# Performance work log

Hardware: AMD Instinct MI355X
Metric: run time of the kernel (lower is better)

The kernel has to match this reference:

```python
import jax, jax.numpy as jnp
import numpy as np

TEMPERATURE = 0.1
B, T, D = 8, 1024, 1024
NEG_INF = -1e30

def setup_inputs() -> dict:
    key = jax.random.key(0)
    k1, k2, k3 = jax.random.split(key, 3)
    features = jax.random.normal(k1, (B, T, D), dtype=jnp.float32)
    masks = jax.random.bernoulli(k2, 0.05, (B, 1, T, T)).astype(jnp.float32)
    input_coords_length = jax.random.randint(k3, (B,), T // 2, T - 1)  # int32
    return {"features": features, "masks": masks, "input_coords_length": input_coords_length}


def _sup_con_loss(feat, mask, L):
    # feat: [T, D], mask: [T, T] float, L: scalar int valid length (slice [:L, :L])
    Tn = feat.shape[0]
    dt = feat.dtype
    vr = jnp.arange(Tn) < L                              # valid rows/cols [T]
    valid2d = (vr[:, None] & vr[None, :]).astype(dt)     # [T, T]
    dot = jnp.matmul(feat, feat.T) / TEMPERATURE         # [T, T]
    dot = jnp.where(vr[None, :], dot, NEG_INF)           # exclude padded cols from max
    logits = dot - jax.lax.stop_gradient(jnp.max(dot, axis=-1, keepdims=True))
    logits_mask = (1.0 - jnp.eye(Tn, dtype=dt)) * valid2d  # off-diagonal, in-slice
    exp_logits = jnp.exp(logits) * logits_mask
    m = mask * valid2d
    # negative_mask = 1-mask; entries < 1 zeroed (binary mask -> indicator of mask==0)
    neg = 1.0 - m
    neg = jnp.where(neg < 1.0, 0.0, neg) * valid2d
    # positive_mask = mask with entries > 0 set to 1
    pos = jnp.where(m > 0, 1.0, m)
    neg_denom = jnp.sum(exp_logits * neg, axis=-1, keepdims=True)
    pos_denom = jax.lax.stop_gradient(jnp.sum(exp_logits * pos, axis=-1, keepdims=True))
    log_prob = logits - jnp.log(neg_denom + pos_denom + 1e-6)
    m2 = m * logits_mask
    mean_log_prob_pos = (m2 * log_prob).sum(-1) / (m2.sum(-1) + 1e-6)  # [T]
    # mean over the L valid rows only (matches .mean() on the sliced tensor)
    return -jnp.sum(jnp.where(vr, mean_log_prob_pos, 0.0)) / L.astype(dt)


def _is_valid(mask, L):
    # valid sample iff sliced mask differs from eye(L) with [0,0]=0
    Tn = mask.shape[0]
    vr = jnp.arange(Tn) < L
    valid2d = (vr[:, None] & vr[None, :]).astype(mask.dtype)
    sanity = jnp.eye(Tn, dtype=mask.dtype).at[0, 0].set(0.0) * valid2d
    return jnp.any((mask * valid2d) != sanity)


def reference(features, masks, input_coords_length):
    L = input_coords_length + 1                      # [B]
    mask0 = masks[:, 0]                              # [B, T, T] (num_layers asserted == 1)
    losses = jax.vmap(_sup_con_loss)(features, mask0, L)   # [B]
    valid = jax.vmap(_is_valid)(mask0, L)                  # [B] bool
    vbs = jnp.maximum(jnp.sum(valid.astype(features.dtype)), 1.0)
    return jnp.sum(losses) / vbs
```

## Files before the change

kernel.cpp:

```cpp
#include <hip/hip_runtime.h>
#include <hip/hip_bf16.h>
#include <stdint.h>

#define T_DIM 1024
#define B_DIM 8

typedef __attribute__((ext_vector_type(8))) short short8;
typedef __attribute__((ext_vector_type(4))) float f32x4;

__device__ inline void gll16(const void* g, void* l) {
  __builtin_amdgcn_global_load_lds((__attribute__((address_space(1))) void*)g,
                                   (__attribute__((address_space(3))) void*)l,
                                   16, 0, 0);
}

__global__ __launch_bounds__(256) void convert_kernel(const float* __restrict__ F,
                                                      __hip_bfloat16* __restrict__ Fb) {
  const int t = blockIdx.x * 256 + threadIdx.x;
  const float4 v = ((const float4*)F)[t];
  union { __hip_bfloat16 h[4]; uint64_t u; } p;
  p.h[0] = __float2bfloat16(v.x);
  p.h[1] = __float2bfloat16(v.y);
  p.h[2] = __float2bfloat16(v.z);
  p.h[3] = __float2bfloat16(v.w);
  ((uint64_t*)Fb)[t] = p.u;
}

__global__ __launch_bounds__(512, 4) void fused_kernel(const __hip_bfloat16* __restrict__ Fb,
                                                       const float* __restrict__ M,
                                                       const int* __restrict__ icl,
                                                       float* __restrict__ part) {
  const int id = blockIdx.x;
  const int b  = id & 7;
  const int rt = (id >> 3) & 7;
  const int ct = id >> 6;
  const int L  = icl[b] + 1;
  if (rt * 128 >= L || ct * 128 >= L) return;

  __shared__ char smem[65536];
  __hip_bfloat16* As = (__hip_bfloat16*)smem;
  __hip_bfloat16* Bs = (__hip_bfloat16*)(smem + 32768);
  float* rp = (float*)smem;
  float* rp_m = rp;
  float* rp_d = rp + 512;
  float* rp_s = rp + 1024;
  float* rp_c = rp + 1536;
  float* rp_b = rp + 2048;

  const __hip_bfloat16* F = Fb + ((size_t)b << 20);
  const int tid  = threadIdx.x;
  const int lane = tid & 63;
  const int wave = tid >> 6;
  const int wrow = (wave >> 2) * 64;
  const int wcol = (wave & 3) * 32;
  const int row0 = rt * 128;
  const int col0 = ct * 128;
  const bool diag = (rt == ct);

  const int fr = lane & 15;
  const int q  = lane >> 4;
  const int sl8 = (q ^ ((fr >> 1) & 3)) * 8;

  const int srow = tid >> 2;
  const int sgk  = (((tid & 3) ^ ((tid >> 3) & 3)) * 8);

  const int gc0 = col0 + wcol + fr;
  const int gc1 = gc0 + 16;

  uint32_t mbits = 0;
  {
    const float* Mb = M + ((size_t)b << 20);
#pragma unroll
    for (int ti = 0; ti < 4; ti++)
#pragma unroll
      for (int r = 0; r < 4; r++) {
        const int grow = row0 + wrow + ti * 16 + q * 4 + r;
        const float* mrow = Mb + ((size_t)grow << 10);
        const uint32_t b0 = (gc0 < L && mrow[gc0] != 0.f) ? 1u : 0u;
        const uint32_t b1 = (gc1 < L && mrow[gc1] != 0.f) ? 1u : 0u;
        mbits |= (b0 << (ti * 8 + r * 2)) | (b1 << (ti * 8 + r * 2 + 1));
      }
  }

  f32x4 acc[4][2];
#pragma unroll
  for (int i = 0; i < 4; i++)
#pragma unroll
    for (int j = 0; j < 2; j++) acc[i][j] = (f32x4){0.f, 0.f, 0.f, 0.f};

  const size_t arow = (size_t)(row0 + srow) * T_DIM + sgk;
  const size_t brow = (size_t)(col0 + srow) * T_DIM + sgk;

  auto stage = [&](int buf, int step) {
    const int kb = step << 6;
#pragma unroll
    for (int p = 0; p < 2; p++)
      gll16(F + arow + kb + p * 32, As + buf * 8192 + p * 4096 + tid * 8);
    if (!diag) {
#pragma unroll
      for (int p = 0; p < 2; p++)
        gll16(F + brow + kb + p * 32, Bs + buf * 8192 + p * 4096 + tid * 8);
    }
  };

  stage(0, 0);
  __syncthreads();

#pragma unroll 2
  for (int t = 0; t < 16; t++) {
    const int cur = t & 1;
    if (t < 15) stage(cur ^ 1, t + 1);
#pragma unroll
    for (int kk = 0; kk < 2; kk++) {
      const __hip_bfloat16* Ab = As + cur * 8192 + kk * 4096;
      const __hip_bfloat16* Bb = diag ? Ab : (Bs + cur * 8192 + kk * 4096);
      short8 af[4], bfr[2];
#pragma unroll
      for (int tt = 0; tt < 4; tt++)
        af[tt] = *(const short8*)(Ab + (wrow + tt * 16 + fr) * 32 + sl8);
#pragma unroll
      for (int j = 0; j < 2; j++)
        bfr[j] = *(const short8*)(Bb + (wcol + j * 16 + fr) * 32 + sl8);
#pragma unroll
      for (int ti = 0; ti < 4; ti++)
#pragma unroll
        for (int tj = 0; tj < 2; tj++)
          acc[ti][tj] = __builtin_amdgcn_mfma_f32_16x16x32_bf16(af[ti], bfr[tj], acc[ti][tj], 0, 0, 0);
    }
    __syncthreads();
  }

#pragma unroll
  for (int ti = 0; ti < 4; ti++) {
#pragma unroll
    for (int r = 0; r < 4; r++) {
      const int lrow = wrow + ti * 16 + q * 4 + r;
      const int grow = row0 + lrow;
      const float mk0 = (float)((mbits >> (ti * 8 + r * 2)) & 1u);
      const float mk1 = (float)((mbits >> (ti * 8 + r * 2 + 1)) & 1u);
      const float s0 = (gc0 < L) ? acc[ti][0][r] * 10.0f : -1e30f;
      const float s1 = (gc1 < L) ? acc[ti][1][r] * 10.0f : -1e30f;
      float m = fmaxf(s0, s1);
#pragma unroll
      for (int d = 1; d < 16; d <<= 1) m = fmaxf(m, __shfl_xor(m, d, 64));
      float den = 0.f, msum = 0.f, cnt = 0.f, badf = 0.f;
      if (gc0 < L) {
        if (gc0 != grow) { den += __expf(s0 - m); msum += mk0 * s0; cnt += mk0; }
        const float sane = (gc0 == grow && grow != 0) ? 1.f : 0.f;
        badf = fmaxf(badf, (mk0 != sane) ? 1.f : 0.f);
      }
      if (gc1 < L) {
        if (gc1 != grow) { den += __expf(s1 - m); msum += mk1 * s1; cnt += mk1; }
        const float sane = (gc1 == grow && grow != 0) ? 1.f : 0.f;
        badf = fmaxf(badf, (mk1 != sane) ? 1.f : 0.f);
      }
#pragma unroll
      for (int d = 1; d < 16; d <<= 1) {
        den  += __shfl_xor(den, d, 64);
        msum += __shfl_xor(msum, d, 64);
        cnt  += __shfl_xor(cnt, d, 64);
        badf  = fmaxf(badf, __shfl_xor(badf, d, 64));
      }
      if (fr == 0) {
        const int slot = wave & 3;
        rp_m[lrow * 4 + slot] = m;   rp_d[lrow * 4 + slot] = den;
        rp_s[lrow * 4 + slot] = msum; rp_c[lrow * 4 + slot] = cnt;
        rp_b[lrow * 4 + slot] = badf;
      }
    }
  }
  __syncthreads();

  if (tid < 128) {
    float m = -1e30f;
#pragma unroll
    for (int s = 0; s < 4; s++) m = fmaxf(m, rp_m[tid * 4 + s]);
    float den = 0.f, msum = 0.f, cnt = 0.f, badf = 0.f;
#pragma unroll
    for (int s = 0; s < 4; s++) {
      den  += rp_d[tid * 4 + s] * __expf(rp_m[tid * 4 + s] - m);
      msum += rp_s[tid * 4 + s];
      cnt  += rp_c[tid * 4 + s];
      badf  = fmaxf(badf, rp_b[tid * 4 + s]);
    }
    float* p = part + ((((size_t)b * 1024 + row0 + tid) * 8) + ct) * 5;
    p[0] = m; p[1] = den; p[2] = msum; p[3] = cnt; p[4] = badf;
  }
}

__global__ __launch_bounds__(256) void reduce_kernel(const float* __restrict__ part,
                                                     const int* __restrict__ icl,
                                                     float* __restrict__ blk_sum,
                                                     int* __restrict__ blk_bad) {
  const int blk = blockIdx.x;
  const int row = blk * 256 + threadIdx.x;
  const int b = row >> 10;
  const int i = row & 1023;
  const int L = icl[b] + 1;
  float rv = 0.f;
  int bad = 0;
  if (i < L) {
    const float* p = part + (size_t)row * 40;
    const int ns = (L + 127) >> 7;
    float m = -1e30f;
    for (int s = 0; s < ns; s++) m = fmaxf(m, p[s * 5 + 0]);
    float den = 0.f, msum = 0.f, cnt = 0.f, badf = 0.f;
    for (int s = 0; s < ns; s++) {
      den  += p[s * 5 + 1] * __expf(p[s * 5 + 0] - m);
      msum += p[s * 5 + 2];
      cnt  += p[s * 5 + 3];
      badf  = fmaxf(badf, p[s * 5 + 4]);
    }
    const float A = msum - cnt * m;
    const float mlpp = (A - cnt * __logf(den + 1e-6f)) / (cnt + 1e-6f);
    rv = -mlpp / (float)L;
    bad = badf > 0.f ? 1 : 0;
  }
  const int tid  = threadIdx.x;
  const int lane = tid & 63;
  const int wave = tid >> 6;
  for (int o = 32; o > 0; o >>= 1) rv += __shfl_down(rv, o, 64);
  const int wbad = (__ballot(bad) != 0ull) ? 1 : 0;
  __shared__ float sred[4];
  __shared__ int bred[4];
  if (lane == 0) { sred[wave] = rv; bred[wave] = wbad; }
  __syncthreads();
  if (tid == 0) {
    blk_sum[blk] = sred[0] + sred[1] + sred[2] + sred[3];
    blk_bad[blk] = bred[0] | bred[1] | bred[2] | bred[3];
  }
}

__global__ __launch_bounds__(64) void final_kernel(const float* __restrict__ blk_sum,
                                                   const int* __restrict__ blk_bad,
                                                   float* __restrict__ out) {
  const int tid = threadIdx.x;
  float v = (tid < 32) ? blk_sum[tid] : 0.f;
  for (int o = 32; o > 0; o >>= 1) v += __shfl_down(v, o, 64);
  if (tid == 0) {
    int vcount = 0;
    for (int bb = 0; bb < B_DIM; bb++) {
      const int any = blk_bad[bb * 4] | blk_bad[bb * 4 + 1] |
                      blk_bad[bb * 4 + 2] | blk_bad[bb * 4 + 3];
      vcount += any ? 1 : 0;
    }
    out[0] = v / fmaxf((float)vcount, 1.0f);
  }
}

extern "C" void kernel_launch(void* const* d_in, const int* in_sizes, int n_in,
                              void* d_out, int out_size, void* d_ws, size_t ws_size,
                              hipStream_t stream) {
  const float* feat = (const float*)d_in[0];
  const float* mask = (const float*)d_in[1];
  const int*   icl  = (const int*)d_in[2];
  float* out = (float*)d_out;

  char* ws = (char*)d_ws;
  __hip_bfloat16* Fb = (__hip_bfloat16*)ws;
  float* part    = (float*)(ws + (16u << 20));
  float* blk_sum = (float*)(ws + (18u << 20));
  int*   blk_bad = (int*)(ws + (18u << 20) + 512);

  convert_kernel<<<dim3(8192), dim3(256), 0, stream>>>(feat, Fb);
  fused_kernel<<<dim3(512), dim3(512), 0, stream>>>(Fb, mask, icl, part);
  reduce_kernel<<<dim3(32), dim3(256), 0, stream>>>(part, icl, blk_sum, blk_bad);
  final_kernel<<<dim3(1), dim3(64), 0, stream>>>(blk_sum, blk_bad, out);
}
```

Before: 139.5 us.

## Restructure GEMM main loop with two-deep prefetch and explicit waitcnt barriers

The K loop now keeps two stages of global-to-LDS loads in flight, uses explicit vmcnt/lgkmcnt waits with raw s_barrier in place of __syncthreads, loads all LDS fragments for a step before issuing MFMAs, and raises wave priority around the MFMA block. The mask loads are issued as raw values before the prefetch so their latency overlaps the first stages. The diagonal-tile shortcut that reused the A tile for B is removed, so diagonal blocks now load B redundantly. This trades simpler code and some extra loads for better latency hiding of memory traffic.

Result: slower. 143.1 us (+2.6%).

```diff
diff --git a/kernel.cpp b/kernel.cpp
--- a/kernel.cpp
+++ b/kernel.cpp
@@ -55,7 +55,6 @@
   const int wcol = (wave & 3) * 32;
   const int row0 = rt * 128;
   const int col0 = ct * 128;
-  const bool diag = (rt == ct);
 
   const int fr = lane & 15;
   const int q  = lane >> 4;
@@ -67,7 +66,7 @@
   const int gc0 = col0 + wcol + fr;
   const int gc1 = gc0 + 16;
 
-  uint32_t mbits = 0;
+  float mv0[16], mv1[16];
   {
     const float* Mb = M + ((size_t)b << 20);
 #pragma unroll
@@ -76,17 +75,10 @@
       for (int r = 0; r < 4; r++) {
         const int grow = row0 + wrow + ti * 16 + q * 4 + r;
         const float* mrow = Mb + ((size_t)grow << 10);
-        const uint32_t b0 = (gc0 < L && mrow[gc0] != 0.f) ? 1u : 0u;
-        const uint32_t b1 = (gc1 < L && mrow[gc1] != 0.f) ? 1u : 0u;
-        mbits |= (b0 << (ti * 8 + r * 2)) | (b1 << (ti * 8 + r * 2 + 1));
-      }
-  }
-
-  f32x4 acc[4][2];
-#pragma unroll
-  for (int i = 0; i < 4; i++)
-#pragma unroll
-    for (int j = 0; j < 2; j++) acc[i][j] = (f32x4){0.f, 0.f, 0.f, 0.f};
+        mv0[ti * 4 + r] = (gc0 < L) ? mrow[gc0] : 0.f;
+        mv1[ti * 4 + r] = (gc1 < L) ? mrow[gc1] : 0.f;
+      }
+  }
 
   const size_t arow = (size_t)(row0 + srow) * T_DIM + sgk;
   const size_t brow = (size_t)(col0 + srow) * T_DIM + sgk;
@@ -96,39 +88,68 @@
 #pragma unroll
     for (int p = 0; p < 2; p++)
       gll16(F + arow + kb + p * 32, As + buf * 8192 + p * 4096 + tid * 8);
-    if (!diag) {
-#pragma unroll
-      for (int p = 0; p < 2; p++)
-        gll16(F + brow + kb + p * 32, Bs + buf * 8192 + p * 4096 + tid * 8);
-    }
+#pragma unroll
+    for (int p = 0; p < 2; p++)
+      gll16(F + brow + kb + p * 32, Bs + buf * 8192 + p * 4096 + tid * 8);
   };
 
   stage(0, 0);
+  stage(1, 1);
+
+  uint32_t mbits = 0;
+#pragma unroll
+  for (int ti = 0; ti < 4; ti++)
+#pragma unroll
+    for (int r = 0; r < 4; r++) {
+      const uint32_t b0 = (mv0[ti * 4 + r] != 0.f) ? 1u : 0u;
+      const uint32_t b1 = (mv1[ti * 4 + r] != 0.f) ? 1u : 0u;
+      mbits |= (b0 << (ti * 8 + r * 2)) | (b1 << (ti * 8 + r * 2 + 1));
+    }
+
+  f32x4 acc[4][2];
+#pragma unroll
+  for (int i = 0; i < 4; i++)
+#pragma unroll
+    for (int j = 0; j < 2; j++) acc[i][j] = (f32x4){0.f, 0.f, 0.f, 0.f};
+
+#pragma unroll
+  for (int t = 0; t < 16; ++t) {
+    const int cur = t & 1;
+    if (t < 15) { asm volatile("s_waitcnt vmcnt(4)" ::: "memory"); }
+    else        { asm volatile("s_waitcnt vmcnt(0)" ::: "memory"); }
+    __builtin_amdgcn_s_barrier();
+    __builtin_amdgcn_sched_barrier(0);
+
+    short8 af[2][4], bfr[2][2];
+    const __hip_bfloat16* Ab = As + cur * 8192;
+    const __hip_bfloat16* Bb = Bs + cur * 8192;
+#pragma unroll
+    for (int kk = 0; kk < 2; kk++) {
+#pragma unroll
+      for (int tt = 0; tt < 4; tt++)
+        af[kk][tt] = *(const short8*)(Ab + kk * 4096 + (wrow + tt * 16 + fr) * 32 + sl8);
+#pragma unroll
+      for (int j = 0; j < 2; j++)
+        bfr[kk][j] = *(const short8*)(Bb + kk * 4096 + (wcol + j * 16 + fr) * 32 + sl8);
+    }
+    asm volatile("s_waitcnt lgkmcnt(0)" ::: "memory");
+    __builtin_amdgcn_sched_barrier(0);
+    __builtin_amdgcn_s_barrier();
+    __builtin_amdgcn_sched_barrier(0);
+
+    if (t < 14) stage(cur, t + 2);
+
+    __builtin_amdgcn_s_setprio(1);
+#pragma unroll
+    for (int kk = 0; kk < 2; kk++)
+#pragma unroll
+      for (int ti = 0; ti < 4; ti++)
+#pragma unroll
+        for (int tj = 0; tj < 2; tj++)
+          acc[ti][tj] = __builtin_amdgcn_mfma_f32_16x16x32_bf16(af[kk][ti], bfr[kk][tj], acc[ti][tj], 0, 0, 0);
+    __builtin_amdgcn_s_setprio(0);
+  }
   __syncthreads();
-
-#pragma unroll 2
-  for (int t = 0; t < 16; t++) {
-    const int cur = t & 1;
-    if (t < 15) stage(cur ^ 1, t + 1);
-#pragma unroll
-    for (int kk = 0; kk < 2; kk++) {
-      const __hip_bfloat16* Ab = As + cur * 8192 + kk * 4096;
-      const __hip_bfloat16* Bb = diag ? Ab : (Bs + cur * 8192 + kk * 4096);
-      short8 af[4], bfr[2];
-#pragma unroll
-      for (int tt = 0; tt < 4; tt++)
-        af[tt] = *(const short8*)(Ab + (wrow + tt * 16 + fr) * 32 + sl8);
-#pragma unroll
-      for (int j = 0; j < 2; j++)
-        bfr[j] = *(const short8*)(Bb + (wcol + j * 16 + fr) * 32 + sl8);
-#pragma unroll
-      for (int ti = 0; ti < 4; ti++)
-#pragma unroll
-        for (int tj = 0; tj < 2; tj++)
-          acc[ti][tj] = __builtin_amdgcn_mfma_f32_16x16x32_bf16(af[ti], bfr[tj], acc[ti][tj], 0, 0, 0);
-    }
-    __syncthreads();
-  }
 
 #pragma unroll
   for (int ti = 0; ti < 4; ti++) {
```
